# Kernel optimization log

Hardware: AMD Instinct MI355X
Metric: run time of the kernel (lower is better)

## Reference

```python
import jax, jax.numpy as jnp
import numpy as np

B, T, D = 16, 4096, 256


def setup_inputs() -> dict:
    key = jax.random.key(0)
    ks = jax.random.split(key, 10)
    s = 1.0 / np.sqrt(D)  # torch nn.Linear default init range
    inp = {
        "x": jax.random.normal(ks[0], (B, T, D), jnp.float32),
        "hidden": jax.random.normal(ks[1], (B, D), jnp.float32),
    }
    names = ["W0", "b0", "W1", "b1", "W2", "b2", "W3", "b3"]
    for i, n in enumerate(names):
        shape = (D, D) if n.startswith("W") else (D,)
        inp[n] = jax.random.uniform(ks[2 + i], shape, jnp.float32, -s, s)
    return inp


def _gln(x, W0, b0, W1, b1, W2, b2, W3, b3):
    # Two gated-linear blocks; the final Linear(hyper[-1], hidden_size) in the
    # original module is never applied by calc_gln (index == len-1 is skipped).
    h = (x @ W0.T + b0) * jax.nn.sigmoid(x @ W1.T + b1)
    return (h @ W2.T + b2) * jax.nn.sigmoid(h @ W3.T + b3)


def reference(x, hidden, W0, b0, W1, b1, W2, b2, W3, b3):
    b = _gln(x, W0, b0, W1, b1, W2, b2, W3, b3)  # [B, T, D]
    bt = jnp.swapaxes(b, 0, 1)  # [T, B, D] for time-major scan
    init = jax.nn.relu(bt[0] + jnp.roll(hidden, 1, -1))

    def step(prev, b_t):
        out = jax.nn.relu(b_t + jnp.roll(prev, 1, -1))
        return out, out

    last, ys = jax.lax.scan(step, init, bt[1:])
    outputs = jnp.concatenate([init[None], ys], axis=0)  # [T, B, D]
    outputs = jnp.swapaxes(outputs, 0, 1)  # [B, T, D]; squeeze(2) is a no-op for D>1
    return outputs, last
```

## Files before the change

### kernel.cpp

```cpp
#include <hip/hip_runtime.h>
#include <hip/hip_bf16.h>
#include <cstdint>
#include <cstddef>

typedef __bf16 bf16x8 __attribute__((ext_vector_type(8)));
typedef float  f32x4  __attribute__((ext_vector_type(4)));

static constexpr int B  = 16;
static constexpr int T  = 4096;
static constexpr int D  = 256;
static constexpr int M  = B * T;
static constexpr int SEGS = 64;
static constexpr int SEGL = T / SEGS;

__global__ void cvt_w(const float* __restrict__ W0, const float* __restrict__ W1,
                      const float* __restrict__ W2, const float* __restrict__ W3,
                      __bf16* __restrict__ wp) {
    int i = blockIdx.x * blockDim.x + threadIdx.x;
    int s    = i >> 14;
    int r    = i & 16383;
    int ks   = r >> 11;
    int fg   = (r >> 6) & 31;
    int lane = r & 63;
    int kg = lane >> 4, rl = lane & 15;
    int w = fg >> 2, f = fg & 3;
    int q = f >> 1, gate = f & 1;
    int rc = w * 32 + 2 * rl + q;
    const float* src = (s == 0) ? (gate ? W1 : W0) : (gate ? W3 : W2);
    const float* p = src + (size_t)rc * 256 + ks * 32 + kg * 8;
    bf16x8 o;
#pragma unroll
    for (int j = 0; j < 8; ++j) o[j] = (__bf16)p[j];
    *reinterpret_cast<bf16x8*>(wp + (size_t)s * 131072 +
                               ((size_t)((ks * 32 + fg) * 64 + lane)) * 8) = o;
}

__launch_bounds__(512, 4)
__global__ void gln_fused(const float* __restrict__ x,
                          const __bf16* __restrict__ wp,
                          const float* __restrict__ b0, const float* __restrict__ b1,
                          const float* __restrict__ b2, const float* __restrict__ b3,
                          float* __restrict__ out) {
    __shared__ char tile[32768];

    const int tid  = threadIdx.x;
    const int lane = tid & 63;
    const int wid  = tid >> 6;
    const int rl   = lane & 15;
    const int kg   = lane >> 4;
    const int row0 = blockIdx.x * 64;

    const __bf16* wv0 = wp + ((size_t)(wid * 4) * 64 + lane) * 8;
    const __bf16* wv1 = wv0 + 131072;

    bf16x8 bbuf[2][4];
    auto loadB = [&](int p, const __bf16* wvb, int ks) {
#pragma unroll
        for (int f = 0; f < 4; ++f)
            bbuf[p][f] = *reinterpret_cast<const bf16x8*>(wvb + ks * 16384 + f * 512);
    };

    {
        int r  = tid >> 3;
        int c0 = tid & 7;
        const float* xr = x + (size_t)(row0 + r) * 256;
        float4 xa[4][2];
#pragma unroll
        for (int ci = 0; ci < 4; ++ci) {
            const float4* p = reinterpret_cast<const float4*>(xr + (c0 + ci * 8) * 8);
            xa[ci][0] = p[0];
            xa[ci][1] = p[1];
        }
#pragma unroll
        for (int ci = 0; ci < 4; ++ci) {
            int ck = c0 + ci * 8;
            int pc = ck ^ ((r & 7) << 2);
            bf16x8 o = { (__bf16)xa[ci][0].x, (__bf16)xa[ci][0].y,
                         (__bf16)xa[ci][0].z, (__bf16)xa[ci][0].w,
                         (__bf16)xa[ci][1].x, (__bf16)xa[ci][1].y,
                         (__bf16)xa[ci][1].z, (__bf16)xa[ci][1].w };
            *reinterpret_cast<bf16x8*>(&tile[r * 512 + pc * 16]) = o;
        }
    }
    loadB(0, wv0, 0);
    __syncthreads();

    f32x4 acc[4][4];

    auto run_stage = [&](const __bf16* wvb) {
#pragma unroll
        for (int m = 0; m < 4; ++m)
#pragma unroll
            for (int f = 0; f < 4; ++f) acc[m][f] = (f32x4){0.f, 0.f, 0.f, 0.f};
#pragma unroll
        for (int ks = 0; ks < 8; ++ks) {
            if (ks < 7) loadB((ks + 1) & 1, wvb, ks + 1);
            bf16x8 aR[4];
#pragma unroll
            for (int m = 0; m < 4; ++m) {
                int row = m * 16 + rl;
                int pc  = (ks * 4 + kg) ^ ((row & 7) << 2);
                aR[m] = *reinterpret_cast<const bf16x8*>(&tile[row * 512 + pc * 16]);
            }
#pragma unroll
            for (int m = 0; m < 4; ++m)
#pragma unroll
                for (int f = 0; f < 4; ++f)
                    acc[m][f] = __builtin_amdgcn_mfma_f32_16x16x32_bf16(
                        aR[m], bbuf[ks & 1][f], acc[m][f], 0, 0, 0);
        }
    };

    const int rc0 = wid * 32 + 2 * rl;

    run_stage(wv0);
    loadB(0, wv1, 0);
    __syncthreads();
    {
        float2 bb0 = *reinterpret_cast<const float2*>(b0 + rc0);
        float2 bb1 = *reinterpret_cast<const float2*>(b1 + rc0);
        int cb  = rc0 * 2;
        int ck  = cb >> 4;
        int off = cb & 15;
#pragma unroll
        for (int m = 0; m < 4; ++m)
#pragma unroll
            for (int j = 0; j < 4; ++j) {
                int row = m * 16 + kg * 4 + j;
                float he = (acc[m][0][j] + bb0.x) *
                           (1.0f / (1.0f + __expf(-(acc[m][1][j] + bb1.x))));
                float ho = (acc[m][2][j] + bb0.y) *
                           (1.0f / (1.0f + __expf(-(acc[m][3][j] + bb1.y))));
                unsigned short ue = __builtin_bit_cast(unsigned short, (__bf16)he);
                unsigned short uo = __builtin_bit_cast(unsigned short, (__bf16)ho);
                unsigned int u = ((unsigned int)uo << 16) | (unsigned int)ue;
                int pc = ck ^ ((row & 7) << 2);
                *reinterpret_cast<unsigned int*>(&tile[row * 512 + pc * 16 + off]) = u;
            }
    }
    __syncthreads();

    run_stage(wv1);
    {
        float2 bb2 = *reinterpret_cast<const float2*>(b2 + rc0);
        float2 bb3 = *reinterpret_cast<const float2*>(b3 + rc0);
#pragma unroll
        for (int m = 0; m < 4; ++m)
#pragma unroll
            for (int j = 0; j < 4; ++j) {
                int row = m * 16 + kg * 4 + j;
                float he = (acc[m][0][j] + bb2.x) *
                           (1.0f / (1.0f + __expf(-(acc[m][1][j] + bb3.x))));
                float ho = (acc[m][2][j] + bb2.y) *
                           (1.0f / (1.0f + __expf(-(acc[m][3][j] + bb3.y))));
                float2 o; o.x = he; o.y = ho;
                *reinterpret_cast<float2*>(out + (size_t)(row0 + row) * 256 + rc0) = o;
            }
    }
}

__global__ void scan_seg(const float* __restrict__ bmat, float2* __restrict__ seg_am) {
    int tid   = blockIdx.x * blockDim.x + threadIdx.x;
    int c     = tid & 255;
    int rest  = tid >> 8;
    int batch = rest & 15;
    int seg   = rest >> 4;
    const float* base = bmat + (size_t)batch * T * D;
    float A = 0.f, Mx = -1e30f;
    int t0 = seg * SEGL;
#pragma unroll 8
    for (int i = 0; i < SEGL; ++i) {
        int t = t0 + i;
        float v = base[(size_t)t * 256 + ((c + t) & 255)];
        A += v;
        Mx = fmaxf(Mx + v, 0.f);
    }
    float2 o; o.x = A; o.y = Mx;
    seg_am[(size_t)(batch * SEGS + seg) * 256 + c] = o;
}

__global__ void scan_bound(const float2* __restrict__ seg_am,
                           const float* __restrict__ hidden,
                           float* __restrict__ seg_state) {
    int tid   = blockIdx.x * blockDim.x + threadIdx.x;
    int c     = tid & 255;
    int batch = tid >> 8;
    float s = hidden[batch * 256 + ((c + 255) & 255)];
    for (int seg = 0; seg < SEGS; ++seg) {
        seg_state[(size_t)(batch * SEGS + seg) * 256 + c] = s;
        float2 am = seg_am[(size_t)(batch * SEGS + seg) * 256 + c];
        s = fmaxf(s + am.x, am.y);
    }
}

__global__ void scan_apply(float* __restrict__ bio,
                           const float* __restrict__ seg_state,
                           float* __restrict__ last) {
    int tid   = blockIdx.x * blockDim.x + threadIdx.x;
    int c     = tid & 255;
    int rest  = tid >> 8;
    int batch = rest & 15;
    int seg   = rest >> 4;
    float s = seg_state[(size_t)(batch * SEGS + seg) * 256 + c];
    float* base = bio + (size_t)batch * T * D;
    int t0 = seg * SEGL;
#pragma unroll 8
    for (int i = 0; i < SEGL; ++i) {
        int t = t0 + i;
        size_t idx = (size_t)t * 256 + ((c + t) & 255);
        float v = base[idx];
        s = fmaxf(s + v, 0.f);
        base[idx] = s;
    }
    if (seg == SEGS - 1) last[batch * 256 + ((c + 255) & 255)] = s;
}

extern "C" void kernel_launch(void* const* d_in, const int* in_sizes, int n_in,
                              void* d_out, int out_size, void* d_ws, size_t ws_size,
                              hipStream_t stream) {
    const float* x      = (const float*)d_in[0];
    const float* hidden = (const float*)d_in[1];
    const float* W0 = (const float*)d_in[2];
    const float* b0 = (const float*)d_in[3];
    const float* W1 = (const float*)d_in[4];
    const float* b1 = (const float*)d_in[5];
    const float* W2 = (const float*)d_in[6];
    const float* b2 = (const float*)d_in[7];
    const float* W3 = (const float*)d_in[8];
    const float* b3 = (const float*)d_in[9];

    float* out  = (float*)d_out;
    float* last = out + (size_t)M * D;

    char* ws = (char*)d_ws;
    __bf16* wpb       = (__bf16*)ws;
    float2* seg_am    = (float2*)(ws + 524288);
    float*  seg_state = (float*)(ws + 524288 + 2097152);

    cvt_w<<<128, 256, 0, stream>>>(W0, W1, W2, W3, wpb);
    gln_fused<<<M / 64, 512, 0, stream>>>(x, wpb, b0, b1, b2, b3, out);

    scan_seg<<<(B * D * SEGS) / 256, 256, 0, stream>>>(out, seg_am);
    scan_bound<<<B * D / 256, 256, 0, stream>>>(seg_am, hidden, seg_state);
    scan_apply<<<(B * D * SEGS) / 256, 256, 0, stream>>>(out, seg_state, last);
}
```

Measured before the change: 95.76 us.

## Fuse segment scan summaries into GEMM epilogue and fold boundary pass into apply

Result: faster. 88.11 us (-8.0%).

```diff
diff --git a/kernel.cpp b/kernel.cpp
--- a/kernel.cpp
+++ b/kernel.cpp
@@ -40,7 +40,8 @@
                           const __bf16* __restrict__ wp,
                           const float* __restrict__ b0, const float* __restrict__ b1,
                           const float* __restrict__ b2, const float* __restrict__ b3,
-                          float* __restrict__ out) {
+                          float* __restrict__ out,
+                          float2* __restrict__ seg_am) {
     __shared__ char tile[32768];
 
     const int tid  = threadIdx.x;
@@ -141,6 +142,8 @@
     __syncthreads();
 
     run_stage(wv1);
+
+    float2 ov[16];
     {
         float2 bb2 = *reinterpret_cast<const float2*>(b2 + rc0);
         float2 bb3 = *reinterpret_cast<const float2*>(b3 + rc0);
@@ -154,54 +157,87 @@
                 float ho = (acc[m][2][j] + bb2.y) *
                            (1.0f / (1.0f + __expf(-(acc[m][3][j] + bb3.y))));
                 float2 o; o.x = he; o.y = ho;
-                *reinterpret_cast<float2*>(out + (size_t)(row0 + row) * 256 + rc0) = o;
+                ov[m * 4 + j] = o;
             }
     }
-}
-
-__global__ void scan_seg(const float* __restrict__ bmat, float2* __restrict__ seg_am) {
-    int tid   = blockIdx.x * blockDim.x + threadIdx.x;
-    int c     = tid & 255;
-    int rest  = tid >> 8;
-    int batch = rest & 15;
-    int seg   = rest >> 4;
-    const float* base = bmat + (size_t)batch * T * D;
+    __syncthreads();
+
+    float* ftile = reinterpret_cast<float*>(tile);
+#pragma unroll
+    for (int m = 0; m < 2; ++m)
+#pragma unroll
+        for (int j = 0; j < 4; ++j) {
+            int row = m * 16 + kg * 4 + j;
+            int col = rc0 ^ ((row & 7) << 2);
+            *reinterpret_cast<float2*>(&ftile[row * 256 + col]) = ov[m * 4 + j];
+        }
+    __syncthreads();
+
+    const int batch = row0 >> 12;
+    const int t0    = row0 & 4095;
+    const int seg   = t0 >> 6;
     float A = 0.f, Mx = -1e30f;
-    int t0 = seg * SEGL;
+    int cc = 0;
+    if (tid < 256) {
+        cc = (tid + t0) & 255;
 #pragma unroll 8
-    for (int i = 0; i < SEGL; ++i) {
-        int t = t0 + i;
-        float v = base[(size_t)t * 256 + ((c + t) & 255)];
-        A += v;
-        Mx = fmaxf(Mx + v, 0.f);
-    }
-    float2 o; o.x = A; o.y = Mx;
-    seg_am[(size_t)(batch * SEGS + seg) * 256 + c] = o;
-}
-
-__global__ void scan_bound(const float2* __restrict__ seg_am,
+        for (int i = 0; i < 32; ++i) {
+            int col = ((cc + i) & 255) ^ ((i & 7) << 2);
+            float v = ftile[i * 256 + col];
+            A += v;
+            Mx = fmaxf(Mx + v, 0.f);
+        }
+    }
+    __syncthreads();
+#pragma unroll
+    for (int m = 2; m < 4; ++m)
+#pragma unroll
+        for (int j = 0; j < 4; ++j) {
+            int row = m * 16 + kg * 4 + j;
+            int pr  = row & 31;
+            int col = rc0 ^ ((pr & 7) << 2);
+            *reinterpret_cast<float2*>(&ftile[pr * 256 + col]) = ov[m * 4 + j];
+        }
+    __syncthreads();
+
+#pragma unroll
+    for (int m = 0; m < 4; ++m)
+#pragma unroll
+        for (int j = 0; j < 4; ++j) {
+            int row = m * 16 + kg * 4 + j;
+            *reinterpret_cast<float2*>(out + (size_t)(row0 + row) * 256 + rc0) =
+                ov[m * 4 + j];
+        }
+
+    if (tid < 256) {
+#pragma unroll 8
+        for (int i = 32; i < 64; ++i) {
+            int pr  = i - 32;
+            int col = ((cc + i) & 255) ^ ((pr & 7) << 2);
+            float v = ftile[pr * 256 + col];
+            A += v;
+            Mx = fmaxf(Mx + v, 0.f);
+        }
+        float2 o; o.x = A; o.y = Mx;
+        seg_am[(size_t)(batch * SEGS + seg) * 256 + tid] = o;
+    }
+}
+
+__global__ void scan_apply(float* __restrict__ bio,
+                           const float2* __restrict__ seg_am,
                            const float* __restrict__ hidden,
-                           float* __restrict__ seg_state) {
-    int tid   = blockIdx.x * blockDim.x + threadIdx.x;
-    int c     = tid & 255;
-    int batch = tid >> 8;
-    float s = hidden[batch * 256 + ((c + 255) & 255)];
-    for (int seg = 0; seg < SEGS; ++seg) {
-        seg_state[(size_t)(batch * SEGS + seg) * 256 + c] = s;
-        float2 am = seg_am[(size_t)(batch * SEGS + seg) * 256 + c];
-        s = fmaxf(s + am.x, am.y);
-    }
-}
-
-__global__ void scan_apply(float* __restrict__ bio,
-                           const float* __restrict__ seg_state,
                            float* __restrict__ last) {
     int tid   = blockIdx.x * blockDim.x + threadIdx.x;
     int c     = tid & 255;
     int rest  = tid >> 8;
     int batch = rest & 15;
     int seg   = rest >> 4;
-    float s = seg_state[(size_t)(batch * SEGS + seg) * 256 + c];
+    float s = hidden[batch * 256 + ((c + 255) & 255)];
+    const float2* am = seg_am + ((size_t)batch * SEGS) * 256 + c;
+    for (int k = 0; k < seg; ++k) {
+        float2 a = am[(size_t)k * 256];
+        s = fmaxf(s + a.x, a.y);
+    }
     float* base = bio + (size_t)batch * T * D;
     int t0 = seg * SEGL;
 #pragma unroll 8
@@ -233,14 +269,10 @@
     float* last = out + (size_t)M * D;
 
     char* ws = (char*)d_ws;
-    __bf16* wpb       = (__bf16*)ws;
-    float2* seg_am    = (float2*)(ws + 524288);
-    float*  seg_state = (float*)(ws + 524288 + 2097152);
+    __bf16* wpb    = (__bf16*)ws;
+    float2* seg_am = (float2*)(ws + 524288);
 
     cvt_w<<<128, 256, 0, stream>>>(W0, W1, W2, W3, wpb);
-    gln_fused<<<M / 64, 512, 0, stream>>>(x, wpb, b0, b1, b2, b3, out);
-
-    scan_seg<<<(B * D * SEGS) / 256, 256, 0, stream>>>(out, seg_am);
-    scan_bound<<<B * D / 256, 256, 0, stream>>>(seg_am, hidden, seg_state);
-    scan_apply<<<(B * D * SEGS) / 256, 256, 0, stream>>>(out, seg_state, last);
-}
+    gln_fused<<<M / 64, 512, 0, stream>>>(x, wpb, b0, b1, b2, b3, out, seg_am);
+    scan_apply<<<(B * D * SEGS) / 256, 256, 0, stream>>>(out, seg_am, hidden, last);
+}
```
